# Kernel optimization log

Hardware: AMD Instinct MI355X
Metric: run time of the kernel (lower is better)

Reference implementation:

```python
import jax, jax.numpy as jnp
import numpy as np

NUM_EXPERTS = 256
TOP_K = 8
N_GROUP = 8
TOPK_GROUP = 4
ROUTED_SCALING = 2.5
HIDDEN = 7168
TOKENS = 16384


def setup_inputs() -> dict:
    key = jax.random.key(0)
    k1, k2, k3 = jax.random.split(key, 3)
    hidden_states = jax.random.normal(k1, (TOKENS, HIDDEN), dtype=jnp.float32)
    weight = jax.random.normal(k2, (NUM_EXPERTS, HIDDEN), dtype=jnp.float32) * 0.02
    e_score_correction_bias = jax.random.normal(k3, (NUM_EXPERTS,), dtype=jnp.float32) * 0.1
    return {
        "hidden_states": hidden_states,
        "weight": weight,
        "e_score_correction_bias": e_score_correction_bias,
    }


def reference(hidden_states, weight, e_score_correction_bias):
    T = hidden_states.shape[0]
    experts_per_group = NUM_EXPERTS // N_GROUP
    # Router logits: [T, num_experts]
    router_logits = jnp.einsum("th,eh->te", hidden_states.astype(jnp.float32), weight)
    scores = jax.nn.sigmoid(router_logits)
    scores_for_choice = scores + e_score_correction_bias  # broadcast over tokens
    # ---- group-limited top-k selection (noaux_tc) ----
    scores_grouped = scores_for_choice.reshape(T, N_GROUP, experts_per_group)
    group_top2, _ = jax.lax.top_k(scores_grouped, 2)           # [T, n_group, 2]
    group_scores = group_top2.sum(axis=-1)                      # [T, n_group]
    _, group_indices = jax.lax.top_k(group_scores, TOPK_GROUP)  # [T, topk_group]
    group_mask = jax.nn.one_hot(group_indices, N_GROUP, dtype=scores.dtype).max(axis=1)  # [T, n_group]
    expert_mask = jnp.broadcast_to(group_mask[:, :, None], (T, N_GROUP, experts_per_group)).reshape(T, NUM_EXPERTS)
    masked_scores = scores_for_choice * expert_mask
    # ---- final expert top-k ----
    _, selected_experts = jax.lax.top_k(masked_scores, TOP_K)   # [T, top_k]
    routing_weights = jnp.take_along_axis(scores, selected_experts, axis=-1)
    # norm_topk_prob
    routing_weights = routing_weights / (routing_weights.sum(axis=-1, keepdims=True) + 1e-20)
    routing_weights = routing_weights * ROUTED_SCALING
    return routing_weights, selected_experts
```

## Files before the change

### kernel.cpp

```cpp
#include <hip/hip_runtime.h>
#include <math.h>
#include <stdint.h>

#define TOKENS 16384
#define HIDDEN 7168
#define NE     256
#define NGROUP 8
#define GSIZE  32
#define TOPKG  4
#define TOPK   8

#define KSPLIT 2
#define TM     128
#define BK     32
#define KC_TOTAL (HIDDEN / BK)
#define KC_SLICE (KC_TOTAL / KSPLIT)

#define WPLANES_BYTES ((size_t)KC_TOTAL * 32 * 1024)

typedef _Float16 half8 __attribute__((ext_vector_type(8)));
typedef float    floatx4 __attribute__((ext_vector_type(4)));
typedef unsigned int u32;
#define GAS __attribute__((address_space(1)))
#define LAS __attribute__((address_space(3)))

__global__ void prep_w(const float* __restrict__ W, _Float16* __restrict__ wp) {
    const int c = blockIdx.x * 128 + threadIdx.x;
    const int e = blockIdx.y;
    const int k = c * 8;
    const float* src = W + (size_t)e * HIDDEN + k;
    float4 v0 = *(const float4*)src;
    float4 v1 = *(const float4*)(src + 4);
    float xv[8] = {v0.x, v0.y, v0.z, v0.w, v1.x, v1.y, v1.z, v1.w};
    half8 h, l;
    #pragma unroll
    for (int j = 0; j < 8; j++) {
        _Float16 hh = (_Float16)xv[j];
        h[j] = hh;
        l[j] = (_Float16)((xv[j] - (float)hh) * 2048.0f);
    }
    const int kc = c >> 2;
    const int g  = c & 3;
    const int lane = g * 16 + (e & 15);
    const int et   = e >> 4;
    const size_t base = (size_t)kc * 16384 + (size_t)et * 512 + (size_t)lane * 8;
    *(half8*)(wp + base)        = h;
    *(half8*)(wp + base + 8192) = l;
}

__global__ __launch_bounds__(512, 2)
void gemm_kernel(const float* __restrict__ X, const _Float16* __restrict__ wp,
                 float* __restrict__ partial) {
    __shared__ __align__(16) _Float16 smem[24576];

    const int tid = threadIdx.x;
    const int b   = blockIdx.x;
    const int mt0 = b >> 1;
    const int ks  = b & 1;
    const int t0  = mt0 * TM;
    const int kc0 = ks * KC_SLICE;

    const int w    = tid >> 6;
    const int lane = tid & 63;
    const int wr   = w & 1;
    const int wc   = w >> 1;

    const int at = tid >> 2;
    const int ac = tid & 3;
    const float* Xrow = X + (size_t)(t0 + at) * HIDDEN + ac * 8;
    const int awoff = (at >> 4) * 512 + (16 * ac + (at & 15)) * 8;

    floatx4 acc0[4][4], acc1[4][4];
    #pragma unroll
    for (int i = 0; i < 4; i++)
        #pragma unroll
        for (int j = 0; j < 4; j++) {
            acc0[i][j] = (floatx4){0.f, 0.f, 0.f, 0.f};
            acc1[i][j] = (floatx4){0.f, 0.f, 0.f, 0.f};
        }

    const char* wbase = (const char*)wp;

    for (int kc = kc0; kc < kc0 + KC_SLICE; kc++) {
        __syncthreads();

        const char* wsrc = wbase + (size_t)kc * 32768;
        char* bdst = (char*)smem + 16384;
        #pragma unroll
        for (int i = 0; i < 4; i++) {
            const int o = (tid + 512 * i) * 16;
            __builtin_amdgcn_global_load_lds((GAS const u32*)(wsrc + o),
                                             (LAS u32*)(bdst + o), 16, 0, 0);
        }

        const float* xp = Xrow + (size_t)kc * BK;
        float4 v0 = *(const float4*)xp;
        float4 v1 = *(const float4*)(xp + 4);
        float xv[8] = {v0.x, v0.y, v0.z, v0.w, v1.x, v1.y, v1.z, v1.w};
        half8 ahh, ahl;
        #pragma unroll
        for (int j = 0; j < 8; j++) {
            _Float16 hh = (_Float16)xv[j];
            ahh[j] = hh;
            ahl[j] = (_Float16)((xv[j] - (float)hh) * 2048.0f);
        }
        *(half8*)(smem + awoff)        = ahh;
        *(half8*)(smem + 4096 + awoff) = ahl;

        __syncthreads();

        const _Float16* Ah = smem + (4 * wr) * 512;
        const _Float16* Bb = smem + 8192 + (4 * wc) * 512;
        half8 bh[4], bl[4];
        #pragma unroll
        for (int et = 0; et < 4; et++) {
            bh[et] = *(const half8*)(Bb + et * 512 + lane * 8);
            bl[et] = *(const half8*)(Bb + 8192 + et * 512 + lane * 8);
        }
        #pragma unroll
        for (int mt = 0; mt < 4; mt++) {
            half8 ah = *(const half8*)(Ah + mt * 512 + lane * 8);
            half8 al = *(const half8*)(Ah + 4096 + mt * 512 + lane * 8);
            #pragma unroll
            for (int et = 0; et < 4; et++) {
                acc0[mt][et] = __builtin_amdgcn_mfma_f32_16x16x32_f16(ah, bh[et], acc0[mt][et], 0, 0, 0);
                acc1[mt][et] = __builtin_amdgcn_mfma_f32_16x16x32_f16(ah, bl[et], acc1[mt][et], 0, 0, 0);
                acc1[mt][et] = __builtin_amdgcn_mfma_f32_16x16x32_f16(al, bh[et], acc1[mt][et], 0, 0, 0);
            }
        }
    }

    float* P = partial + (size_t)ks * TOKENS * NE;
    const int rbase0 = t0 + 64 * wr;
    const int cbase0 = 64 * wc;
    const float inv = 1.0f / 2048.0f;
    #pragma unroll
    for (int mt = 0; mt < 4; mt++)
        #pragma unroll
        for (int et = 0; et < 4; et++) {
            floatx4 r = acc0[mt][et] + acc1[mt][et] * inv;
            const int col = cbase0 + 16 * et + (lane & 15);
            const int row = rbase0 + 16 * mt + (lane >> 4) * 4;
            #pragma unroll
            for (int rr = 0; rr < 4; rr++)
                P[(size_t)(row + rr) * NE + col] = r[rr];
        }
}

__global__ __launch_bounds__(64)
void select_kernel(const float* __restrict__ partial, const float* __restrict__ bias,
                   float* __restrict__ out) {
    __shared__ float sfc[32][257];
    const int tid = threadIdx.x;
    const int t0  = blockIdx.x * 32;
    const float* P0 = partial;
    const float* P1 = partial + (size_t)TOKENS * NE;

    for (int t = 0; t < 32; t++) {
        #pragma unroll
        for (int e0 = 0; e0 < NE; e0 += 64) {
            const int e = e0 + tid;
            const size_t idx = (size_t)(t0 + t) * NE + e;
            const float logit = P0[idx] + P1[idx];
            const float sig = 1.0f / (1.0f + expf(-logit));
            sfc[t][e] = sig + bias[e];
        }
    }
    __syncthreads();

    if (tid < 32) {
        float* s = sfc[tid];
        float gs[NGROUP];
        #pragma unroll
        for (int g = 0; g < NGROUP; g++) {
            float m1 = -INFINITY, m2 = -INFINITY;
            for (int x = 0; x < GSIZE; x++) {
                const float v = s[g * GSIZE + x];
                if (v > m1) { m2 = m1; m1 = v; }
                else if (v > m2) { m2 = v; }
            }
            gs[g] = m1 + m2;
        }
        bool gsel[NGROUP] = {false,false,false,false,false,false,false,false};
        for (int r = 0; r < TOPKG; r++) {
            int bi = 0; float bv = -INFINITY;
            for (int g = 0; g < NGROUP; g++)
                if (!gsel[g] && gs[g] > bv) { bv = gs[g]; bi = g; }
            gsel[bi] = true;
        }
        int sel[TOPK]; float wgt[TOPK]; float sum = 0.f;
        for (int r = 0; r < TOPK; r++) {
            int bi = 0; float bv = -INFINITY;
            for (int e = 0; e < NE; e++) {
                const float sv = s[e];
                const float v = (sv == -INFINITY) ? -INFINITY
                               : (gsel[e >> 5] ? sv : 0.0f);
                if (v > bv) { bv = v; bi = e; }
            }
            sel[r] = bi;
            wgt[r] = s[bi] - bias[bi];
            s[bi]  = -INFINITY;
            sum += wgt[r];
        }
        const float scale = 2.5f / (sum + 1e-20f);
        const int gt = t0 + tid;
        #pragma unroll
        for (int r = 0; r < TOPK; r++) {
            out[(size_t)gt * TOPK + r] = wgt[r] * scale;
            out[(size_t)TOKENS * TOPK + (size_t)gt * TOPK + r] = (float)sel[r];
        }
    }
}

extern "C" void kernel_launch(void* const* d_in, const int* in_sizes, int n_in,
                              void* d_out, int out_size, void* d_ws, size_t ws_size,
                              hipStream_t stream) {
    const float* X  = (const float*)d_in[0];
    const float* W  = (const float*)d_in[1];
    const float* eb = (const float*)d_in[2];
    float* out = (float*)d_out;

    _Float16* wp   = (_Float16*)d_ws;
    float* partial = (float*)((char*)d_ws + WPLANES_BYTES);

    hipLaunchKernelGGL(prep_w, dim3(7, 256), dim3(128), 0, stream, W, wp);
    hipLaunchKernelGGL(gemm_kernel, dim3(TM == 128 ? 256 : 256), dim3(512), 0, stream, X, wp, partial);
    hipLaunchKernelGGL(select_kernel, dim3(TOKENS / 32), dim3(64), 0, stream, partial, eb, out);
}
```

Measured before the change: 821.3 us.

## Shrink GEMM token tile to 64, prefetch X a step ahead, widen select

Halves the GEMM token tile so each 256-thread block covers 64 tokens across all 256 experts, giving twice as many blocks. The next X chunk is prefetched into registers during the MFMA work, and the MFMA order is regrouped by accumulator. The select kernel's logit/sigmoid load phase now uses 256 threads instead of 64. The risk is that weight tiles are reloaded per smaller token tile, roughly doubling weight traffic per FLOP.

```diff
diff --git a/kernel.cpp b/kernel.cpp
--- a/kernel.cpp
+++ b/kernel.cpp
@@ -11,7 +11,7 @@
 #define TOPK   8
 
 #define KSPLIT 2
-#define TM     128
+#define TM     64
 #define BK     32
 #define KC_TOTAL (HIDDEN / BK)
 #define KC_SLICE (KC_TOTAL / KSPLIT)
@@ -27,8 +27,7 @@
 __global__ void prep_w(const float* __restrict__ W, _Float16* __restrict__ wp) {
     const int c = blockIdx.x * 128 + threadIdx.x;
     const int e = blockIdx.y;
-    const int k = c * 8;
-    const float* src = W + (size_t)e * HIDDEN + k;
+    const float* src = W + (size_t)e * HIDDEN + c * 8;
     float4 v0 = *(const float4*)src;
     float4 v1 = *(const float4*)(src + 4);
     float xv[8] = {v0.x, v0.y, v0.z, v0.w, v1.x, v1.y, v1.z, v1.w};
@@ -48,27 +47,26 @@
     *(half8*)(wp + base + 8192) = l;
 }
 
-__global__ __launch_bounds__(512, 2)
+__global__ __launch_bounds__(256, 2)
 void gemm_kernel(const float* __restrict__ X, const _Float16* __restrict__ wp,
                  float* __restrict__ partial) {
-    __shared__ __align__(16) _Float16 smem[24576];
-
-    const int tid = threadIdx.x;
-    const int b   = blockIdx.x;
-    const int mt0 = b >> 1;
-    const int ks  = b & 1;
-    const int t0  = mt0 * TM;
-    const int kc0 = ks * KC_SLICE;
+    __shared__ __align__(16) _Float16 smem[20480];
+
+    const int tid  = threadIdx.x;
+    const int b    = blockIdx.x;
+    const int tb   = b >> 1;
+    const int ks   = b & 1;
+    const int t0   = tb * TM;
 
     const int w    = tid >> 6;
     const int lane = tid & 63;
-    const int wr   = w & 1;
-    const int wc   = w >> 1;
 
     const int at = tid >> 2;
     const int ac = tid & 3;
-    const float* Xrow = X + (size_t)(t0 + at) * HIDDEN + ac * 8;
-    const int awoff = (at >> 4) * 512 + (16 * ac + (at & 15)) * 8;
+    const int awoff = (at >> 4) * 512 + (ac * 16 + (at & 15)) * 8;
+    const float* Xrow = X + (size_t)(t0 + at) * HIDDEN + ks * (HIDDEN / KSPLIT) + ac * 8;
+
+    const char* wbase = (const char*)wp + (size_t)ks * KC_SLICE * 32768;
 
     floatx4 acc0[4][4], acc1[4][4];
     #pragma unroll
@@ -79,38 +77,45 @@
             acc1[i][j] = (floatx4){0.f, 0.f, 0.f, 0.f};
         }
 
-    const char* wbase = (const char*)wp;
-
-    for (int kc = kc0; kc < kc0 + KC_SLICE; kc++) {
+    float4 v0 = *(const float4*)Xrow;
+    float4 v1 = *(const float4*)(Xrow + 4);
+
+    for (int i = 0; i < KC_SLICE; i++) {
         __syncthreads();
 
-        const char* wsrc = wbase + (size_t)kc * 32768;
-        char* bdst = (char*)smem + 16384;
-        #pragma unroll
-        for (int i = 0; i < 4; i++) {
-            const int o = (tid + 512 * i) * 16;
-            __builtin_amdgcn_global_load_lds((GAS const u32*)(wsrc + o),
-                                             (LAS u32*)(bdst + o), 16, 0, 0);
-        }
-
-        const float* xp = Xrow + (size_t)kc * BK;
-        float4 v0 = *(const float4*)xp;
-        float4 v1 = *(const float4*)(xp + 4);
-        float xv[8] = {v0.x, v0.y, v0.z, v0.w, v1.x, v1.y, v1.z, v1.w};
-        half8 ahh, ahl;
-        #pragma unroll
-        for (int j = 0; j < 8; j++) {
-            _Float16 hh = (_Float16)xv[j];
-            ahh[j] = hh;
-            ahl[j] = (_Float16)((xv[j] - (float)hh) * 2048.0f);
-        }
-        *(half8*)(smem + awoff)        = ahh;
-        *(half8*)(smem + 4096 + awoff) = ahl;
+        {
+            float xv[8] = {v0.x, v0.y, v0.z, v0.w, v1.x, v1.y, v1.z, v1.w};
+            half8 ahh, ahl;
+            #pragma unroll
+            for (int j = 0; j < 8; j++) {
+                _Float16 hh = (_Float16)xv[j];
+                ahh[j] = hh;
+                ahl[j] = (_Float16)((xv[j] - (float)hh) * 2048.0f);
+            }
+            *(half8*)(smem + awoff)        = ahh;
+            *(half8*)(smem + 2048 + awoff) = ahl;
+        }
+
+        {
+            const char* wsrc = wbase + (size_t)i * 32768;
+            char* bdst = (char*)(smem + 4096);
+            #pragma unroll
+            for (int q = 0; q < 8; q++) {
+                const int o = (tid + 256 * q) * 16;
+                __builtin_amdgcn_global_load_lds((GAS const u32*)(wsrc + o),
+                                                 (LAS u32*)(bdst + o), 16, 0, 0);
+            }
+        }
 
         __syncthreads();
 
-        const _Float16* Ah = smem + (4 * wr) * 512;
-        const _Float16* Bb = smem + 8192 + (4 * wc) * 512;
+        if (i + 1 < KC_SLICE) {
+            const float* xp = Xrow + (size_t)(i + 1) * BK;
+            v0 = *(const float4*)xp;
+            v1 = *(const float4*)(xp + 4);
+        }
+
+        const _Float16* Bb = smem + 4096 + w * 2048;
         half8 bh[4], bl[4];
         #pragma unroll
         for (int et = 0; et < 4; et++) {
@@ -119,35 +124,36 @@
         }
         #pragma unroll
         for (int mt = 0; mt < 4; mt++) {
-            half8 ah = *(const half8*)(Ah + mt * 512 + lane * 8);
-            half8 al = *(const half8*)(Ah + 4096 + mt * 512 + lane * 8);
-            #pragma unroll
-            for (int et = 0; et < 4; et++) {
+            half8 ah = *(const half8*)(smem + mt * 512 + lane * 8);
+            half8 al = *(const half8*)(smem + 2048 + mt * 512 + lane * 8);
+            #pragma unroll
+            for (int et = 0; et < 4; et++)
                 acc0[mt][et] = __builtin_amdgcn_mfma_f32_16x16x32_f16(ah, bh[et], acc0[mt][et], 0, 0, 0);
+            #pragma unroll
+            for (int et = 0; et < 4; et++)
                 acc1[mt][et] = __builtin_amdgcn_mfma_f32_16x16x32_f16(ah, bl[et], acc1[mt][et], 0, 0, 0);
+            #pragma unroll
+            for (int et = 0; et < 4; et++)
                 acc1[mt][et] = __builtin_amdgcn_mfma_f32_16x16x32_f16(al, bh[et], acc1[mt][et], 0, 0, 0);
-            }
         }
     }
 
     float* P = partial + (size_t)ks * TOKENS * NE;
-    const int rbase0 = t0 + 64 * wr;
-    const int cbase0 = 64 * wc;
     const float inv = 1.0f / 2048.0f;
     #pragma unroll
     for (int mt = 0; mt < 4; mt++)
         #pragma unroll
         for (int et = 0; et < 4; et++) {
             floatx4 r = acc0[mt][et] + acc1[mt][et] * inv;
-            const int col = cbase0 + 16 * et + (lane & 15);
-            const int row = rbase0 + 16 * mt + (lane >> 4) * 4;
+            const int col = w * 64 + 16 * et + (lane & 15);
+            const int row = t0 + 16 * mt + (lane >> 4) * 4;
             #pragma unroll
             for (int rr = 0; rr < 4; rr++)
                 P[(size_t)(row + rr) * NE + col] = r[rr];
         }
 }
 
-__global__ __launch_bounds__(64)
+__global__ __launch_bounds__(256)
 void select_kernel(const float* __restrict__ partial, const float* __restrict__ bias,
                    float* __restrict__ out) {
     __shared__ float sfc[32][257];
@@ -156,15 +162,13 @@
     const float* P0 = partial;
     const float* P1 = partial + (size_t)TOKENS * NE;
 
-    for (int t = 0; t < 32; t++) {
-        #pragma unroll
-        for (int e0 = 0; e0 < NE; e0 += 64) {
-            const int e = e0 + tid;
-            const size_t idx = (size_t)(t0 + t) * NE + e;
-            const float logit = P0[idx] + P1[idx];
-            const float sig = 1.0f / (1.0f + expf(-logit));
-            sfc[t][e] = sig + bias[e];
-        }
+    for (int idx = tid; idx < 32 * NE; idx += 256) {
+        const int t = idx >> 8;
+        const int e = idx & 255;
+        const size_t g = (size_t)(t0 + t) * NE + e;
+        const float logit = P0[g] + P1[g];
+        const float sig = 1.0f / (1.0f + expf(-logit));
+        sfc[t][e] = sig + bias[e];
     }
     __syncthreads();
 
@@ -224,6 +228,6 @@
     float* partial = (float*)((char*)d_ws + WPLANES_BYTES);
 
     hipLaunchKernelGGL(prep_w, dim3(7, 256), dim3(128), 0, stream, W, wp);
-    hipLaunchKernelGGL(gemm_kernel, dim3(TM == 128 ? 256 : 256), dim3(512), 0, stream, X, wp, partial);
-    hipLaunchKernelGGL(select_kernel, dim3(TOKENS / 32), dim3(64), 0, stream, partial, eb, out);
-}
+    hipLaunchKernelGGL(gemm_kernel, dim3(TOKENS / TM * KSPLIT), dim3(256), 0, stream, X, wp, partial);
+    hipLaunchKernelGGL(select_kernel, dim3(TOKENS / 32), dim3(256), 0, stream, partial, eb, out);
+}
```

After: 784.6 us. 4.5% less time.
